# Kernel optimization log

Hardware: AMD Instinct MI355X
Metric: run time of the kernel (lower is better)

The kernel has to match this reference:

```python
import jax, jax.numpy as jnp
import numpy as np

B = 8192      # number of molecules (graphs)
T = 524288    # total flat candidates (avg 64 per graph, jagged)
D = 128       # embed_dim
V = 100000    # unique templates (table has V+1 rows incl. 'unknown')


def setup_inputs() -> dict:
    key = jax.random.key(0)
    k1, k2, k3 = jax.random.split(key, 3)
    rng = np.random.default_rng(0)
    # jagged lengths, each segment >= 1, summing exactly to T
    lengths = rng.multinomial(T - B, np.ones(B) / B) + 1
    seg_ids = np.repeat(np.arange(B), lengths)           # [T], sorted segment ids
    offsets = np.concatenate([[0], np.cumsum(lengths)[:-1]])
    target_pos = offsets + rng.integers(0, lengths)      # one target per segment
    return {
        "graph_embed": jax.random.normal(k1, (B, D), dtype=jnp.float32),
        "tpl_embedding": jax.random.normal(k2, (V + 1, D), dtype=jnp.float32),
        "cand_idx": jax.random.randint(k3, (T,), 0, V + 1),
        "seg_ids": jnp.asarray(seg_ids, dtype=jnp.int32),
        "target_pos": jnp.asarray(target_pos, dtype=jnp.int32),
    }


def reference(graph_embed, tpl_embedding, cand_idx, seg_ids, target_pos):
    num_seg = graph_embed.shape[0]
    # gather candidate (template) embeddings: [T, D]
    cand_embed = tpl_embedding[cand_idx]
    # gather graph embedding per candidate (torch.gather with rep_indices): [T, D]
    g = graph_embed[seg_ids]
    # inner-product attention score per candidate: [T]
    logits = jnp.sum(g * cand_embed, axis=1)
    # jagged (segment-wise) log-softmax over variable-length candidate lists
    seg_max = jax.ops.segment_max(logits, seg_ids, num_segments=num_seg)
    shifted = logits - seg_max[seg_ids]
    seg_sum = jax.ops.segment_sum(jnp.exp(shifted), seg_ids, num_segments=num_seg)
    log_prob = shifted - jnp.log(seg_sum)[seg_ids]
    # gather the log-prob of the target template per graph: [B]
    return log_prob[target_pos]
```

## Files before the change

kernel.cpp:

```cpp
#include <hip/hip_runtime.h>
#include <hip/hip_fp16.h>

#define D 128
#define LOG2E 1.4426950408889634f
#define LN2   0.6931471805599453f

__global__ __launch_bounds__(256) void prep_kernel(
    const float4* __restrict__ tpl_src,
    uint2* __restrict__ tpl_dst,
    const int* __restrict__ seg_ids,
    int* __restrict__ seg_start,
    int nt4, int T, int B)
{
    const int stride = gridDim.x * blockDim.x;
    const int tid0 = blockIdx.x * blockDim.x + threadIdx.x;

    for (int i = tid0; i < nt4; i += stride) {
        const float4 v = tpl_src[i];
        const __half2 h01 = __float22half2_rn(make_float2(v.x, v.y));
        const __half2 h23 = __float22half2_rn(make_float2(v.z, v.w));
        uint2 o;
        o.x = *reinterpret_cast<const unsigned*>(&h01);
        o.y = *reinterpret_cast<const unsigned*>(&h23);
        tpl_dst[i] = o;
    }
    for (int t = tid0; t < T; t += stride) {
        if (t == 0) seg_start[0] = 0;
        else if (seg_ids[t] != seg_ids[t - 1]) seg_start[seg_ids[t]] = t;
        if (t == T - 1) seg_start[B] = T;
    }
}

__global__ __launch_bounds__(256) void fused_kernel(
    const float* __restrict__ graph_embed,
    const __half* __restrict__ tpl_h,
    const int* __restrict__ cand_idx,
    const int* __restrict__ seg_start,
    const int* __restrict__ target_pos,
    float* __restrict__ out,
    int B)
{
    const int sl   = threadIdx.x & 15;
    const int q    = threadIdx.x >> 4;
    const int lseg = q >> 2;
    const int part = q & 3;
    const int b    = blockIdx.x * 4 + lseg;
    if (b >= B) return;

    const int start = seg_start[b];
    const int end   = seg_start[b + 1];
    const int tp    = target_pos[b];

    const float4* grow = (const float4*)(graph_embed + (size_t)b * D);
    const float4 ga = grow[sl * 2];
    const float4 gb = grow[sl * 2 + 1];

    float mA = -3.0e38f, sA = 0.0f;
    float mB = -3.0e38f, sB = 0.0f;
    float tgt = -3.0e38f;

    auto body = [&](int t, float& m, float& s) {
        const int c = cand_idx[t];
        const uint4 xr = ((const uint4*)(tpl_h + (size_t)c * D))[sl];
        const __half2* xh = (const __half2*)&xr;
        const float2 f0 = __half22float2(xh[0]);
        const float2 f1 = __half22float2(xh[1]);
        const float2 f2 = __half22float2(xh[2]);
        const float2 f3 = __half22float2(xh[3]);
        float p = ga.x * f0.x;
        p = fmaf(ga.y, f0.y, p);
        p = fmaf(ga.z, f1.x, p);
        p = fmaf(ga.w, f1.y, p);
        p = fmaf(gb.x, f2.x, p);
        p = fmaf(gb.y, f2.y, p);
        p = fmaf(gb.z, f3.x, p);
        p = fmaf(gb.w, f3.y, p);
        #pragma unroll
        for (int off = 8; off >= 1; off >>= 1) p += __shfl_xor(p, off);
        p *= LOG2E;
        if (t == tp) tgt = p;
        const float M = fmaxf(m, p);
        s = fmaf(s, exp2f(m - M), exp2f(p - M));
        m = M;
    };

    int t = start + part;
    for (; t + 4 < end; t += 8) {
        body(t, mA, sA);
        body(t + 4, mB, sB);
    }
    if (t < end) body(t, mA, sA);

    const float Mq = fmaxf(mA, mB);
    const float Sq = sA * exp2f(mA - Mq) + sB * exp2f(mB - Mq);

    __shared__ float sm[16], ss[16], st[16];
    if (sl == 0) { sm[q] = Mq; ss[q] = Sq; st[q] = tgt; }
    __syncthreads();

    if (threadIdx.x < 4) {
        const int bo = blockIdx.x * 4 + threadIdx.x;
        if (bo < B) {
            const int base = threadIdx.x * 4;
            float M = -3.0e38f;
            #pragma unroll
            for (int j = 0; j < 4; ++j) M = fmaxf(M, sm[base + j]);
            float S = 0.0f, Tg = -3.0e38f;
            #pragma unroll
            for (int j = 0; j < 4; ++j) {
                S += ss[base + j] * exp2f(sm[base + j] - M);
                Tg = fmaxf(Tg, st[base + j]);
            }
            out[bo] = (Tg - M - log2f(S)) * LN2;
        }
    }
}

__global__ void seg_bounds_kernel(const int* __restrict__ seg_ids,
                                  int* __restrict__ seg_start,
                                  int T, int B) {
    int t = blockIdx.x * blockDim.x + threadIdx.x;
    if (t >= T) return;
    if (t == 0) seg_start[0] = 0;
    else if (seg_ids[t] != seg_ids[t - 1]) seg_start[seg_ids[t]] = t;
    if (t == T - 1) seg_start[B] = T;
}

__global__ __launch_bounds__(256) void logits_kernel(
    const float* __restrict__ graph_embed,
    const float* __restrict__ tpl_embedding,
    const int* __restrict__ cand_idx,
    const int* __restrict__ seg_ids,
    float* __restrict__ logits,
    int T)
{
    const int sl  = threadIdx.x & 31;
    const int hw  = (blockIdx.x * blockDim.x + threadIdx.x) >> 5;
    const int nhw = (gridDim.x * blockDim.x) >> 5;

    for (int t0 = hw; t0 < T; t0 += 2 * nhw) {
        const int t1 = t0 + nhw;
        const bool has1 = (t1 < T);
        const int c0 = cand_idx[t0];
        const int s0 = seg_ids[t0];
        const int c1 = has1 ? cand_idx[t1] : c0;
        const int s1 = has1 ? seg_ids[t1] : s0;

        const float4 x0 = ((const float4*)(tpl_embedding + (size_t)c0 * D))[sl];
        const float4 g0 = ((const float4*)(graph_embed   + (size_t)s0 * D))[sl];
        const float4 x1 = ((const float4*)(tpl_embedding + (size_t)c1 * D))[sl];
        const float4 g1 = ((const float4*)(graph_embed   + (size_t)s1 * D))[sl];

        float p0 = fmaf(g0.x, x0.x, fmaf(g0.y, x0.y, fmaf(g0.z, x0.z, g0.w * x0.w)));
        float p1 = fmaf(g1.x, x1.x, fmaf(g1.y, x1.y, fmaf(g1.z, x1.z, g1.w * x1.w)));

        #pragma unroll
        for (int off = 16; off >= 1; off >>= 1) {
            p0 += __shfl_xor(p0, off);
            p1 += __shfl_xor(p1, off);
        }
        if (sl == 0) {
            logits[t0] = p0;
            if (has1) logits[t1] = p1;
        }
    }
}

__global__ __launch_bounds__(256) void seg_reduce_kernel(
    const float* __restrict__ logits,
    const int* __restrict__ seg_start,
    const int* __restrict__ target_pos,
    float* __restrict__ out,
    int B)
{
    const int wave = threadIdx.x >> 6;
    const int lane = threadIdx.x & 63;
    const int b    = blockIdx.x * 4 + wave;
    if (b >= B) return;

    const int start = seg_start[b];
    const int end   = seg_start[b + 1];

    float m = -3.0e38f;
    float s = 0.0f;

    for (int t = start + lane; t < end; t += 64) {
        const float x = logits[t] * LOG2E;
        if (x <= m) {
            s += exp2f(x - m);
        } else {
            s = fmaf(s, exp2f(m - x), 1.0f);
            m = x;
        }
    }

    #pragma unroll
    for (int off = 32; off >= 1; off >>= 1) {
        const float m2 = __shfl_xor(m, off);
        const float s2 = __shfl_xor(s, off);
        const float M  = fmaxf(m, m2);
        s = s * exp2f(m - M) + s2 * exp2f(m2 - M);
        m = M;
    }

    if (lane == 0) {
        const float tl = logits[target_pos[b]] * LOG2E;
        out[b] = (tl - m - log2f(s)) * LN2;
    }
}

extern "C" void kernel_launch(void* const* d_in, const int* in_sizes, int n_in,
                              void* d_out, int out_size, void* d_ws, size_t ws_size,
                              hipStream_t stream) {
    const float* graph_embed   = (const float*)d_in[0];
    const float* tpl_embedding = (const float*)d_in[1];
    const int*   cand_idx      = (const int*)d_in[2];
    const int*   seg_ids       = (const int*)d_in[3];
    const int*   target_pos    = (const int*)d_in[4];
    float*       out           = (float*)d_out;

    const int BE = in_sizes[0];
    const int B  = BE / D;
    const int VE = in_sizes[1];
    const int T  = in_sizes[2];

    size_t off = 0;
    auto alloc = [&](size_t bytes) {
        void* p = (char*)d_ws + off;
        off += (bytes + 255) & ~(size_t)255;
        return p;
    };
    int*    seg_start = (int*)   alloc((size_t)(B + 1) * 4);
    __half* tpl_h     = (__half*)alloc((size_t)VE * 2);
    float*  logits    = (float*) alloc((size_t)T * 4);

    if (off <= ws_size) {
        prep_kernel<<<2048, 256, 0, stream>>>((const float4*)tpl_embedding,
                                              (uint2*)tpl_h,
                                              seg_ids, seg_start,
                                              VE / 4, T, B);
        fused_kernel<<<(B + 3) / 4, 256, 0, stream>>>(graph_embed, tpl_h,
                                                      cand_idx, seg_start,
                                                      target_pos, out, B);
    } else {
        seg_bounds_kernel<<<(T + 255) / 256, 256, 0, stream>>>(seg_ids, seg_start, T, B);
        logits_kernel<<<2048, 256, 0, stream>>>(graph_embed, tpl_embedding,
                                                cand_idx, seg_ids, logits, T);
        seg_reduce_kernel<<<(B + 3) / 4, 256, 0, stream>>>(logits, seg_start,
                                                           target_pos, out, B);
    }
}
```

Measured before the change: 118.1 us.

## Bucket candidates by template-table slice in shared memory before gathering

Each block now counting-sorts its four segments' candidates into 16 buckets by the high bits of the template index. It builds the histogram, prefix sum and scatter with shared-memory atomics, then has each wave process its segment bucket by bucket. The aim is better L2/MALL locality for the random fp16 template-row gathers, since concurrently running waves tend to touch the same slice of the table. In exchange it adds a sort pass with atomics, extra barriers and shared-memory use that may lower occupancy, and the online-softmax reduction moves from shared memory to wave shuffles.

```diff
diff --git a/kernel.cpp b/kernel.cpp
--- a/kernel.cpp
+++ b/kernel.cpp
@@ -4,6 +4,9 @@
 #define D 128
 #define LOG2E 1.4426950408889634f
 #define LN2   0.6931471805599453f
+#define SLSH   13
+#define NSL    16
+#define SEGCAP 512
 
 __global__ __launch_bounds__(256) void prep_kernel(
     const float4* __restrict__ tpl_src,
@@ -38,82 +41,126 @@
     const int* __restrict__ seg_start,
     const int* __restrict__ target_pos,
     float* __restrict__ out,
-    int B)
+    int B, int nsl)
 {
-    const int sl   = threadIdx.x & 15;
-    const int q    = threadIdx.x >> 4;
-    const int lseg = q >> 2;
-    const int part = q & 3;
-    const int b    = blockIdx.x * 4 + lseg;
-    if (b >= B) return;
-
-    const int start = seg_start[b];
-    const int end   = seg_start[b + 1];
-    const int tp    = target_pos[b];
-
-    const float4* grow = (const float4*)(graph_embed + (size_t)b * D);
-    const float4 ga = grow[sl * 2];
-    const float4 gb = grow[sl * 2 + 1];
-
-    float mA = -3.0e38f, sA = 0.0f;
-    float mB = -3.0e38f, sB = 0.0f;
-    float tgt = -3.0e38f;
-
-    auto body = [&](int t, float& m, float& s) {
-        const int c = cand_idx[t];
-        const uint4 xr = ((const uint4*)(tpl_h + (size_t)c * D))[sl];
-        const __half2* xh = (const __half2*)&xr;
-        const float2 f0 = __half22float2(xh[0]);
-        const float2 f1 = __half22float2(xh[1]);
-        const float2 f2 = __half22float2(xh[2]);
-        const float2 f3 = __half22float2(xh[3]);
-        float p = ga.x * f0.x;
-        p = fmaf(ga.y, f0.y, p);
-        p = fmaf(ga.z, f1.x, p);
-        p = fmaf(ga.w, f1.y, p);
-        p = fmaf(gb.x, f2.x, p);
-        p = fmaf(gb.y, f2.y, p);
-        p = fmaf(gb.z, f3.x, p);
-        p = fmaf(gb.w, f3.y, p);
+    __shared__ int2 ent[4 * SEGCAP];
+    __shared__ int  hist[4][NSL];
+    __shared__ int  sbase[4][NSL];
+    __shared__ int  scnt[4][NSL];
+
+    const int tid = threadIdx.x;
+    const int b0  = blockIdx.x * 4;
+
+    if (tid < 4 * NSL) ((int*)hist)[tid] = 0;
+    __syncthreads();
+
+    for (int ls = 0; ls < 4; ++ls) {
+        const int b = b0 + ls;
+        if (b >= B) continue;
+        const int st  = seg_start[b];
+        const int len = min(seg_start[b + 1] - st, SEGCAP);
+        for (int j = tid; j < len; j += 256)
+            atomicAdd(&hist[ls][cand_idx[st + j] >> SLSH], 1);
+    }
+    __syncthreads();
+
+    if (tid < 64) {
+        const int ls = tid >> 4, sl = tid & 15;
+        const int v = hist[ls][sl];
+        int sum = v;
         #pragma unroll
-        for (int off = 8; off >= 1; off >>= 1) p += __shfl_xor(p, off);
-        p *= LOG2E;
-        if (t == tp) tgt = p;
-        const float M = fmaxf(m, p);
-        s = fmaf(s, exp2f(m - M), exp2f(p - M));
+        for (int off = 1; off < 16; off <<= 1) {
+            const int up = __shfl_up(sum, off);
+            if ((tid & 15) >= off) sum += up;
+        }
+        sbase[ls][sl] = sum - v;
+        scnt[ls][sl]  = v;
+        hist[ls][sl]  = 0;
+    }
+    __syncthreads();
+
+    for (int ls = 0; ls < 4; ++ls) {
+        const int b = b0 + ls;
+        if (b >= B) continue;
+        const int st  = seg_start[b];
+        const int len = min(seg_start[b + 1] - st, SEGCAP);
+        for (int j = tid; j < len; j += 256) {
+            const int c  = cand_idx[st + j];
+            const int sl = c >> SLSH;
+            const int r  = atomicAdd(&hist[ls][sl], 1);
+            ent[ls * SEGCAP + sbase[ls][sl] + r] = make_int2(c, st + j);
+        }
+    }
+    __syncthreads();
+
+    const int wls  = tid >> 6;
+    const int lane = tid & 63;
+    const int q    = lane >> 4;
+    const int sl16 = lane & 15;
+    const int b    = b0 + wls;
+
+    float m = -3.0e38f, s = 0.0f, tgt = -3.0e38f;
+
+    if (b < B) {
+        const int st  = seg_start[b];
+        const int end = seg_start[b + 1];
+        const int tp  = target_pos[b];
+
+        const float4* grow = (const float4*)(graph_embed + (size_t)b * D);
+        const float4 ga = grow[sl16 * 2];
+        const float4 gb = grow[sl16 * 2 + 1];
+
+        auto dotupd = [&](int c, int t) {
+            const uint4 xr = ((const uint4*)(tpl_h + (size_t)c * D))[sl16];
+            const __half2* xh = (const __half2*)&xr;
+            const float2 f0 = __half22float2(xh[0]);
+            const float2 f1 = __half22float2(xh[1]);
+            const float2 f2 = __half22float2(xh[2]);
+            const float2 f3 = __half22float2(xh[3]);
+            float p = ga.x * f0.x;
+            p = fmaf(ga.y, f0.y, p);
+            p = fmaf(ga.z, f1.x, p);
+            p = fmaf(ga.w, f1.y, p);
+            p = fmaf(gb.x, f2.x, p);
+            p = fmaf(gb.y, f2.y, p);
+            p = fmaf(gb.z, f3.x, p);
+            p = fmaf(gb.w, f3.y, p);
+            #pragma unroll
+            for (int off = 8; off >= 1; off >>= 1) p += __shfl_xor(p, off);
+            p *= LOG2E;
+            if (t == tp) tgt = p;
+            const float M = fmaxf(m, p);
+            s = fmaf(s, exp2f(m - M), exp2f(p - M));
+            m = M;
+        };
+
+        #pragma unroll 1
+        for (int ps = 0; ps < nsl; ++ps) {
+            const int n  = scnt[wls][ps];
+            const int bs = wls * SEGCAP + sbase[wls][ps];
+            for (int i = q; i < n; i += 4) {
+                const int2 e = ent[bs + i];
+                dotupd(e.x, e.y);
+            }
+        }
+        for (int t0 = st + SEGCAP; t0 < end; t0 += 4) {
+            const int t = t0 + q;
+            if (t < end) dotupd(cand_idx[t], t);
+        }
+    }
+
+    #pragma unroll
+    for (int off = 16; off <= 32; off <<= 1) {
+        const float m2 = __shfl_xor(m, off);
+        const float s2 = __shfl_xor(s, off);
+        const float M  = fmaxf(m, m2);
+        s = s * exp2f(m - M) + s2 * exp2f(m2 - M);
         m = M;
-    };
-
-    int t = start + part;
-    for (; t + 4 < end; t += 8) {
-        body(t, mA, sA);
-        body(t + 4, mB, sB);
-    }
-    if (t < end) body(t, mA, sA);
-
-    const float Mq = fmaxf(mA, mB);
-    const float Sq = sA * exp2f(mA - Mq) + sB * exp2f(mB - Mq);
-
-    __shared__ float sm[16], ss[16], st[16];
-    if (sl == 0) { sm[q] = Mq; ss[q] = Sq; st[q] = tgt; }
-    __syncthreads();
-
-    if (threadIdx.x < 4) {
-        const int bo = blockIdx.x * 4 + threadIdx.x;
-        if (bo < B) {
-            const int base = threadIdx.x * 4;
-            float M = -3.0e38f;
-            #pragma unroll
-            for (int j = 0; j < 4; ++j) M = fmaxf(M, sm[base + j]);
-            float S = 0.0f, Tg = -3.0e38f;
-            #pragma unroll
-            for (int j = 0; j < 4; ++j) {
-                S += ss[base + j] * exp2f(sm[base + j] - M);
-                Tg = fmaxf(Tg, st[base + j]);
-            }
-            out[bo] = (Tg - M - log2f(S)) * LN2;
-        }
-    }
+        tgt = fmaxf(tgt, __shfl_xor(tgt, off));
+    }
+
+    if (b < B && lane == 0)
+        out[b] = (tgt - m - log2f(s)) * LN2;
 }
 
 __global__ void seg_bounds_kernel(const int* __restrict__ seg_ids,
@@ -222,7 +269,10 @@
     const int BE = in_sizes[0];
     const int B  = BE / D;
     const int VE = in_sizes[1];
+    const int V1 = VE / D;
     const int T  = in_sizes[2];
+
+    const int nsl = (V1 + (1 << SLSH) - 1) >> SLSH;
 
     size_t off = 0;
     auto alloc = [&](size_t bytes) {
@@ -234,14 +284,14 @@
     __half* tpl_h     = (__half*)alloc((size_t)VE * 2);
     float*  logits    = (float*) alloc((size_t)T * 4);
 
-    if (off <= ws_size) {
+    if (off <= ws_size && nsl <= NSL) {
         prep_kernel<<<2048, 256, 0, stream>>>((const float4*)tpl_embedding,
                                               (uint2*)tpl_h,
                                               seg_ids, seg_start,
                                               VE / 4, T, B);
         fused_kernel<<<(B + 3) / 4, 256, 0, stream>>>(graph_embed, tpl_h,
                                                       cand_idx, seg_start,
-                                                      target_pos, out, B);
+                                                      target_pos, out, B, nsl);
     } else {
         seg_bounds_kernel<<<(T + 255) / 256, 256, 0, stream>>>(seg_ids, seg_start, T, B);
         logits_kernel<<<2048, 256, 0, stream>>>(graph_embed, tpl_embedding,
```

Measured after the change: 122.3 us. +3.6%, slower.
